# Kernel tuning notes

Measured on AMD Instinct MI355X. Metric: run time of the kernel, lower is better.

The kernel has to match this reference:

```python
import jax, jax.numpy as jnp
import numpy as np

B, L, K = 4096, 4096, 10


def _sparsemax(z):
    # z: [..., n]; Martins & Astudillo sparsemax along last dim
    n = z.shape[-1]
    zs = -jnp.sort(-z, axis=-1)                      # descending
    cum = jnp.cumsum(zs, axis=-1)
    r = jnp.arange(1, n + 1, dtype=z.dtype)
    support = (1.0 + r * zs) > cum                   # [..., n]
    ksel = jnp.sum(support, axis=-1, keepdims=True)  # support size
    tau = (jnp.take_along_axis(cum, ksel - 1, axis=-1) - 1.0) / ksel.astype(z.dtype)
    return jnp.maximum(z - tau, 0.0)


def _topk_bitvectors(logits, k):
    # k highest-scoring binary vectors z in {0,1}^L under <z, logits>
    # (faithful to the CPU batched_topk: detached logits)
    lg = jax.lax.stop_gradient(logits)
    b, latent = lg.shape
    base = (lg > 0).astype(lg.dtype)                 # argmax config [B, L]
    costs = jnp.abs(lg)                              # flip costs
    neg_small, pos = jax.lax.top_k(-costs, k)        # k smallest costs + positions
    c_small = -neg_small                             # [B, k]
    m = 1 << k                                       # 2^k candidate flip subsets
    bits = ((jnp.arange(m)[:, None] >> jnp.arange(k)[None, :]) & 1).astype(lg.dtype)  # [2^k, k]
    sums = jnp.einsum('mk,bk->bm', bits, c_small)    # total flip cost per subset
    _, best = jax.lax.top_k(-sums, k)                # k cheapest subsets [B, k]
    flips = bits[best]                               # [B, k, k] which small-cost bits to flip
    base_at = jnp.take_along_axis(base, pos, axis=1) # base bit value at flip positions [B, k]
    delta = flips * (1.0 - 2.0 * base_at[:, None, :])  # +1 or -1 where flipped
    bv = jnp.broadcast_to(base[:, None, :], (b, k, latent))
    bidx = jnp.arange(b)[:, None, None]
    cidx = jnp.arange(k)[None, :, None]
    jpos = pos[:, None, :]                           # [B, 1, k]
    bv = bv.at[bidx, cidx, jpos].add(delta)          # scatter flips -> [B, k, L]
    return bv


def reference(logits, k):
    bv = _topk_bitvectors(logits, k)                         # [B, k, L]
    scores = jnp.einsum('bkj,bj->bk', bv, logits)            # [B, k]
    distr = _sparsemax(scores)                               # [B, k]
    p = distr.reshape(-1)
    safe_p = jnp.where(p > 0, p, 1.0)
    entropy = -jnp.sum(jnp.where(p > 0, p * jnp.log(safe_p), 0.0))
    batch_size = logits.shape[0]
    return bv, distr, entropy / batch_size


def setup_inputs() -> dict:
    key = jax.random.key(0)
    logits = jax.random.normal(key, (B, L), dtype=jnp.float32)
    return {"logits": logits, "k": K}
```

## Files before the change

kernel.cpp:

```cpp
#include <hip/hip_runtime.h>
#include <stdint.h>

#define NB   4096
#define LDIM 4096
#define KK   10
#define TPB  256
#define CAP  1024

__device__ __forceinline__ unsigned long long wave_min_u64(unsigned long long v) {
#pragma unroll
    for (int off = 1; off < 64; off <<= 1) {
        const unsigned long long o = __shfl_xor(v, off, 64);
        if (o < v) v = o;
    }
    return v;
}

__global__ __launch_bounds__(TPB) void topk_sparsemax(
    const float* __restrict__ logits,
    float* __restrict__ bv,
    float* __restrict__ distr,
    float* __restrict__ ent)
{
    __shared__ float s_wsum[4];
    __shared__ int   s_pos[KK];
    __shared__ int   s_sign[KK];
    __shared__ int   s_bestm[KK];
    __shared__ int   s_cnt;
    __shared__ unsigned long long s_cand[CAP];

    const int b    = blockIdx.x;
    const int t    = threadIdx.x;
    const int lane = t & 63;
    const int wv   = t >> 6;
    const float* __restrict__ row = logits + (size_t)b * LDIM;

    float vals[16];
#pragma unroll
    for (int q = 0; q < 4; q++) {
        const float4 f = *(const float4*)(row + (q << 10) + (t << 2));
        vals[q*4+0] = f.x; vals[q*4+1] = f.y; vals[q*4+2] = f.z; vals[q*4+3] = f.w;
    }

    float s0 = 0.f;
#pragma unroll
    for (int i = 0; i < 16; i++) s0 += vals[i] > 0.f ? vals[i] : 0.f;
#pragma unroll
    for (int off = 1; off < 64; off <<= 1) s0 += __shfl_xor(s0, off, 64);
    if (lane == 0) s_wsum[wv] = s0;

    float T = 0.02f;
    int cnt = 0;
    for (int attempt = 0; attempt < 15; attempt++) {
        if (t == 0) s_cnt = 0;
        __syncthreads();
#pragma unroll
        for (int i = 0; i < 16; i++) {
            const float v    = vals[i];
            const float cost = fabsf(v);
            if (cost < T) {
                const int idx = ((i >> 2) << 10) + (t << 2) + (i & 3);
                const unsigned long long pk =
                    ((unsigned long long)__float_as_uint(cost) << 32)
                    | (unsigned)((idx << 1) | (v > 0.f ? 1 : 0));
                const int p = atomicAdd(&s_cnt, 1);
                if (p < CAP) s_cand[p] = pk;
            }
        }
        __syncthreads();
        cnt = s_cnt;
        if (cnt >= KK && cnt <= CAP) break;
        T = (cnt < KK) ? T * 4.0f : T * 0.25f;
        __syncthreads();
    }

    float4 base4[4];
#pragma unroll
    for (int q = 0; q < 4; q++) {
        base4[q].x = vals[q*4+0] > 0.f ? 1.f : 0.f;
        base4[q].y = vals[q*4+1] > 0.f ? 1.f : 0.f;
        base4[q].z = vals[q*4+2] > 0.f ? 1.f : 0.f;
        base4[q].w = vals[q*4+3] > 0.f ? 1.f : 0.f;
    }
    float* out0 = bv + (size_t)b * (KK * LDIM);
#pragma unroll
    for (int c = 0; c < KK; c++) {
        float* orow = out0 + c * LDIM + (t << 2);
#pragma unroll
        for (int q = 0; q < 4; q++)
            *(float4*)(orow + (q << 10)) = base4[q];
    }

    if (wv == 0) {
        const float S0 = (s_wsum[0] + s_wsum[1]) + (s_wsum[2] + s_wsum[3]);
        float csm[KK];
        unsigned long long prev = 0ull;

        if (cnt >= KK && cnt <= CAP) {
            const int nc = cnt;
#pragma unroll
            for (int c = 0; c < KK; c++) {
                unsigned long long best = ~0ull;
                for (int p = lane; p < nc; p += 64) {
                    const unsigned long long pk = s_cand[p];
                    if ((c == 0 || pk > prev) && pk < best) best = pk;
                }
                best = wave_min_u64(best);
                prev = best;
                csm[c] = __uint_as_float((unsigned)(best >> 32));
                if (lane == 0) {
                    const unsigned lo = (unsigned)best;
                    s_pos[c]  = (int)(lo >> 1);
                    s_sign[c] = (int)(lo & 1u);
                }
            }
        } else {
#pragma unroll
            for (int c = 0; c < KK; c++) {
                unsigned long long best = ~0ull;
                for (int p = lane; p < LDIM; p += 64) {
                    const float v    = row[p];
                    const float cost = fabsf(v);
                    const unsigned long long pk =
                        ((unsigned long long)__float_as_uint(cost) << 32)
                        | (unsigned)((p << 1) | (v > 0.f ? 1 : 0));
                    if ((c == 0 || pk > prev) && pk < best) best = pk;
                }
                best = wave_min_u64(best);
                prev = best;
                csm[c] = __uint_as_float((unsigned)(best >> 32));
                if (lane == 0) {
                    const unsigned lo = (unsigned)best;
                    s_pos[c]  = (int)(lo >> 1);
                    s_sign[c] = (int)(lo & 1u);
                }
            }
        }

        float sums[16];
#pragma unroll
        for (int i = 0; i < 16; i++) {
            const int m = (lane << 4) | i;
            float acc = 0.f;
#pragma unroll
            for (int j = 0; j < KK; j++) acc += (m & (1 << j)) ? csm[j] : 0.f;
            sums[i] = acc;
        }

        float zc[KK];
        unsigned long long prev2 = 0ull;
#pragma unroll
        for (int c = 0; c < KK; c++) {
            unsigned long long best = ~0ull;
#pragma unroll
            for (int i = 0; i < 16; i++) {
                const unsigned long long pk =
                    ((unsigned long long)__float_as_uint(sums[i]) << 32)
                    | (unsigned)((lane << 4) | i);
                if ((c == 0 || pk > prev2) && pk < best) best = pk;
            }
            best = wave_min_u64(best);
            prev2 = best;
            zc[c] = S0 - __uint_as_float((unsigned)(best >> 32));
            if (lane == 0) s_bestm[c] = (int)((unsigned)best & 1023u);
        }

        if (lane == 0) {
            float acc = 0.f; int ks = 0;
#pragma unroll
            for (int r = 1; r <= KK; r++) {
                acc += zc[r-1];
                if (1.f + (float)r * zc[r-1] > acc) ks++;
            }
            float acc2 = 0.f;
#pragma unroll
            for (int r = 0; r < KK; r++) if (r < ks) acc2 += zc[r];
            const float tau = (acc2 - 1.f) / (float)ks;
            float entl = 0.f;
            float* drow = distr + b * KK;
#pragma unroll
            for (int c = 0; c < KK; c++) {
                float p = zc[c] - tau;
                p = p > 0.f ? p : 0.f;
                drow[c] = p;
                if (p > 0.f) entl -= p * logf(p);
            }
            atomicAdd(ent, entl * (1.0f / (float)NB));
        }
    }

    __syncthreads();
    if (t < KK * KK) {
        const int c = t / KK, j = t % KK;
        if ((s_bestm[c] >> j) & 1)
            out0[c * LDIM + s_pos[j]] = s_sign[j] ? 0.f : 1.f;
    }
}

extern "C" void kernel_launch(void* const* d_in, const int* in_sizes, int n_in,
                              void* d_out, int out_size, void* d_ws, size_t ws_size,
                              hipStream_t stream)
{
    const float* logits = (const float*)d_in[0];
    float* out   = (float*)d_out;
    float* bv    = out;
    float* distr = out + (size_t)NB * KK * LDIM;
    float* ent   = distr + (size_t)NB * KK;
    hipMemsetAsync(ent, 0, sizeof(float), stream);
    topk_sparsemax<<<dim3(NB), dim3(TPB), 0, stream>>>(logits, bv, distr, ent);
}
```

Baseline: 718.0 us.

## Write final bitvectors once with nontemporal stores and deterministic entropy reduction

Moves the bitvector output writes after the top-k selection and folds the flip values into registers, so each output element is written once with its final value. This removes the separate scattered second-pass writes to global memory, and the stores are now nontemporal. The single-float atomic entropy accumulation becomes per-row workspace writes plus a small reduction kernel, replacing the memset when the workspace is large enough. In exchange, the big store phase now waits for wave 0's selection work instead of overlapping with it, and a second kernel launch is added.

```diff
diff --git a/kernel.cpp b/kernel.cpp
--- a/kernel.cpp
+++ b/kernel.cpp
@@ -7,6 +7,8 @@
 #define TPB  256
 #define CAP  1024
 
+typedef float fx4 __attribute__((ext_vector_type(4)));
+
 __device__ __forceinline__ unsigned long long wave_min_u64(unsigned long long v) {
 #pragma unroll
     for (int off = 1; off < 64; off <<= 1) {
@@ -20,7 +22,8 @@
     const float* __restrict__ logits,
     float* __restrict__ bv,
     float* __restrict__ distr,
-    float* __restrict__ ent)
+    float* __restrict__ entws,
+    const int entmode)
 {
     __shared__ float s_wsum[4];
     __shared__ int   s_pos[KK];
@@ -74,23 +77,6 @@
         __syncthreads();
     }
 
-    float4 base4[4];
-#pragma unroll
-    for (int q = 0; q < 4; q++) {
-        base4[q].x = vals[q*4+0] > 0.f ? 1.f : 0.f;
-        base4[q].y = vals[q*4+1] > 0.f ? 1.f : 0.f;
-        base4[q].z = vals[q*4+2] > 0.f ? 1.f : 0.f;
-        base4[q].w = vals[q*4+3] > 0.f ? 1.f : 0.f;
-    }
-    float* out0 = bv + (size_t)b * (KK * LDIM);
-#pragma unroll
-    for (int c = 0; c < KK; c++) {
-        float* orow = out0 + c * LDIM + (t << 2);
-#pragma unroll
-        for (int q = 0; q < 4; q++)
-            *(float4*)(orow + (q << 10)) = base4[q];
-    }
-
     if (wv == 0) {
         const float S0 = (s_wsum[0] + s_wsum[1]) + (s_wsum[2] + s_wsum[3]);
         float csm[KK];
@@ -185,16 +171,67 @@
                 drow[c] = p;
                 if (p > 0.f) entl -= p * logf(p);
             }
-            atomicAdd(ent, entl * (1.0f / (float)NB));
+            if (entmode) entws[b] = entl;
+            else         atomicAdd(entws, entl * (1.0f / (float)NB));
         }
     }
 
     __syncthreads();
-    if (t < KK * KK) {
-        const int c = t / KK, j = t % KK;
-        if ((s_bestm[c] >> j) & 1)
-            out0[c * LDIM + s_pos[j]] = s_sign[j] ? 0.f : 1.f;
-    }
+
+    unsigned fm[KK];
+#pragma unroll
+    for (int j = 0; j < KK; j++) {
+        unsigned m = 0u;
+#pragma unroll
+        for (int c = 0; c < KK; c++)
+            m |= (((unsigned)s_bestm[c] >> j) & 1u) << c;
+        fm[j] = m;
+    }
+    int posr[KK], sgnr[KK];
+#pragma unroll
+    for (int j = 0; j < KK; j++) { posr[j] = s_pos[j]; sgnr[j] = s_sign[j]; }
+
+    unsigned rowflip[16]; float flipval[16]; float basef[16];
+#pragma unroll
+    for (int i = 0; i < 16; i++) {
+        const int col = ((i >> 2) << 10) + (t << 2) + (i & 3);
+        unsigned rf = 0u; float fv = 0.f;
+#pragma unroll
+        for (int j = 0; j < KK; j++) {
+            if (posr[j] == col) { rf = fm[j]; fv = sgnr[j] ? 0.f : 1.f; }
+        }
+        rowflip[i] = rf; flipval[i] = fv;
+        basef[i]   = vals[i] > 0.f ? 1.f : 0.f;
+    }
+
+    float* out0 = bv + (size_t)b * (KK * LDIM);
+#pragma unroll
+    for (int c = 0; c < KK; c++) {
+        float* orow = out0 + c * LDIM + (t << 2);
+#pragma unroll
+        for (int q = 0; q < 4; q++) {
+            fx4 v;
+            v.x = ((rowflip[q*4+0] >> c) & 1u) ? flipval[q*4+0] : basef[q*4+0];
+            v.y = ((rowflip[q*4+1] >> c) & 1u) ? flipval[q*4+1] : basef[q*4+1];
+            v.z = ((rowflip[q*4+2] >> c) & 1u) ? flipval[q*4+2] : basef[q*4+2];
+            v.w = ((rowflip[q*4+3] >> c) & 1u) ? flipval[q*4+3] : basef[q*4+3];
+            __builtin_nontemporal_store(v, (fx4*)(orow + (q << 10)));
+        }
+    }
+}
+
+__global__ __launch_bounds__(256) void ent_reduce(
+    const float* __restrict__ ws, float* __restrict__ ent)
+{
+    __shared__ float sw[4];
+    const int t = threadIdx.x, lane = t & 63, wv = t >> 6;
+    float s = 0.f;
+    for (int i = t; i < NB; i += 256) s += ws[i];
+#pragma unroll
+    for (int off = 1; off < 64; off <<= 1) s += __shfl_xor(s, off, 64);
+    if (lane == 0) sw[wv] = s;
+    __syncthreads();
+    if (t == 0) *ent = (sw[0] + sw[1] + sw[2] + sw[3]) * (1.0f / (float)NB);
 }
 
 extern "C" void kernel_launch(void* const* d_in, const int* in_sizes, int n_in,
@@ -206,6 +243,14 @@
     float* bv    = out;
     float* distr = out + (size_t)NB * KK * LDIM;
     float* ent   = distr + (size_t)NB * KK;
-    hipMemsetAsync(ent, 0, sizeof(float), stream);
-    topk_sparsemax<<<dim3(NB), dim3(TPB), 0, stream>>>(logits, bv, distr, ent);
-}
+
+    if (ws_size >= (size_t)NB * sizeof(float)) {
+        topk_sparsemax<<<dim3(NB), dim3(TPB), 0, stream>>>(
+            logits, bv, distr, (float*)d_ws, 1);
+        ent_reduce<<<dim3(1), dim3(256), 0, stream>>>((const float*)d_ws, ent);
+    } else {
+        (void)hipMemsetAsync(ent, 0, sizeof(float), stream);
+        topk_sparsemax<<<dim3(NB), dim3(TPB), 0, stream>>>(
+            logits, bv, distr, ent, 0);
+    }
+}
```

Result: no change. 723.6 us (+0.8%).
